# Kernel tuning notes

Hardware: AMD Instinct MI355X
Metric: run time of the kernel (lower is better)

Reference implementation:

```python
import jax, jax.numpy as jnp
import numpy as np

ALPHA = 0.2          # LeakyReLU negative slope
NEG_INF = -9e15      # mask value from the original code


def setup_inputs() -> dict:
    key = jax.random.key(0)
    k1, k2, k3, k4 = jax.random.split(key, 4)
    B, N, F_in, F_out = 8, 2048, 64, 64
    x = jax.random.normal(k1, (B, N, F_in), dtype=jnp.float32)
    adj = jax.random.randint(k2, (B, N, N), 0, 2, dtype=jnp.int32)
    W = jax.random.normal(k3, (F_in, F_out), dtype=jnp.float32)
    a = jax.random.normal(k4, (2 * F_out, 1), dtype=jnp.float32)
    return {"x": x, "adj": adj, "W": W, "a": a}


def reference(x, adj, W, a):
    # h: [B, N, F_out]
    h = jnp.matmul(x, W)
    F_out = W.shape[1]
    a1 = a[:F_out, 0]   # source half of attention vector
    a2 = a[F_out:, 0]   # target half
    # e_ij = leakyrelu(h_i . a1 + h_j . a2)  -- identical math to the
    # original cat([h_i, h_j]) @ a without materializing [B,N*N,2F].
    s1 = jnp.einsum('bnf,f->bn', h, a1)  # [B, N]
    s2 = jnp.einsum('bnf,f->bn', h, a2)  # [B, N]
    e = jax.nn.leaky_relu(s1[:, :, None] + s2[:, None, :], negative_slope=ALPHA)
    masked = jnp.where(adj > 0, e, NEG_INF)
    attention = jax.nn.softmax(masked, axis=2)  # [B, N, N]
    # dropout p=0.0 / eval mode -> identity
    h_prime = jnp.matmul(attention, h)          # [B, N, F_out]
    return jax.nn.elu(h_prime)                  # concat=True branch
```

## Files before the change

### kernel.cpp

```cpp
#include <hip/hip_runtime.h>
#include <cstdint>

#define LRELU_ALPHA 0.2f
#define NEG_INF -9000000000000000.0f
#define L2E 1.4426950408889634f

typedef __bf16 bf16x8 __attribute__((ext_vector_type(8)));
typedef float floatx4 __attribute__((ext_vector_type(4)));

constexpr int Bb = 8, Nn = 2048, Ff = 64;
constexpr int TJ = 64;
constexpr int SEG = 8;
constexpr int SEGJ = Nn / SEG;
constexpr int NROWS = Bb * Nn;
constexpr int LSTR = 264;

__device__ __forceinline__ unsigned f2bf_u(float f) {
    unsigned u = __builtin_bit_cast(unsigned, f);
    return u + 0x7FFFu + ((u >> 16) & 1u);
}
__device__ __forceinline__ unsigned short f2bf(float f) {
    return (unsigned short)(f2bf_u(f) >> 16);
}
__device__ __forceinline__ unsigned pkbf(float lo, float hi) {
    return (f2bf_u(lo) >> 16) | (f2bf_u(hi) & 0xFFFF0000u);
}

__global__ __launch_bounds__(256) void gat_pack(
    const int* __restrict__ adj, unsigned long long* __restrict__ amask)
{
    const int lane = threadIdx.x & 63;
    const int w    = threadIdx.x >> 6;
    const long long wave_id = (long long)blockIdx.x * 4 + w;
    const long long c0 = wave_id * 16;
    #pragma unroll
    for (int it = 0; it < 16; ++it) {
        const long long chunk = c0 + it;
        const int4 v = reinterpret_cast<const int4*>(adj + chunk * 256)[lane];
        const unsigned long long b0 = __ballot(v.x > 0);
        const unsigned long long b1 = __ballot(v.y > 0);
        const unsigned long long b2 = __ballot(v.z > 0);
        const unsigned long long b3 = __ballot(v.w > 0);
        if (lane == 0) {
            ulonglong2* o = reinterpret_cast<ulonglong2*>(amask + chunk * 4);
            o[0] = ulonglong2{b0, b1};
            o[1] = ulonglong2{b2, b3};
        }
    }
}

__global__ __launch_bounds__(256) void gat_prep(
    const float* __restrict__ x, const float* __restrict__ W, const float* __restrict__ a,
    unsigned short* __restrict__ hT, float* __restrict__ s1g, float* __restrict__ s2g)
{
    constexpr int STR2 = 36;
    __shared__ unsigned short hblk[64 * STR2];
    const int tid = threadIdx.x;
    const int blk = blockIdx.x;
    const int b  = blk >> 6;
    const int i0 = (blk & 63) * 32;
    const int w    = tid >> 6;
    const int lane = tid & 63;

    float wcol[64];
    #pragma unroll
    for (int k = 0; k < 64; ++k) wcol[k] = W[k * 64 + lane];
    const float a1 = a[lane], a2 = a[64 + lane];

    for (int r = 0; r < 8; ++r) {
        const int il = w * 8 + r;
        const int i  = i0 + il;
        const float* xrow = x + ((size_t)(b * Nn + i)) * 64;
        float h = 0.f;
        #pragma unroll
        for (int k = 0; k < 64; ++k) h = fmaf(xrow[k], wcol[k], h);
        float p1 = h * a1, p2 = h * a2;
        #pragma unroll
        for (int off = 32; off; off >>= 1) {
            p1 += __shfl_xor(p1, off);
            p2 += __shfl_xor(p2, off);
        }
        if (lane == 0) { s1g[b * Nn + i] = p1 * L2E; s2g[b * Nn + i] = p2 * L2E; }
        hblk[lane * STR2 + il] = f2bf(h);
    }
    __syncthreads();
    {
        const int f = tid >> 2, c = (tid & 3) * 8;
        uint4 v = *reinterpret_cast<const uint4*>(&hblk[f * STR2 + c]);
        *reinterpret_cast<uint4*>(hT + ((size_t)b * 64 + f) * Nn + i0 + c) = v;
    }
}

__global__ __launch_bounds__(256, 4) void gat_attn(
    const unsigned long long* __restrict__ amask, const unsigned short* __restrict__ hT,
    const float* __restrict__ s1g, const float* __restrict__ s2g,
    float* __restrict__ m_part, float* __restrict__ l_part, float* __restrict__ O_part)
{
    __shared__ unsigned short hT_lds[64 * LSTR];
    __shared__ float s2_lds[SEGJ];

    const int tid  = threadIdx.x;
    const int blk  = blockIdx.x;
    const int seg  = blk >> 8;
    const int grp  = blk & 255;
    const int gr0  = grp * 64;
    const int b    = gr0 >> 11;
    const int i0   = gr0 & 2047;
    const int w    = tid >> 6;
    const int lane = tid & 63;
    const int fl   = lane & 15;
    const int q    = lane >> 4;

    const int i = i0 + w * 16 + fl;
    const float s1v = s1g[b * Nn + i];
    const unsigned short* hTb = hT + (size_t)b * 64 * Nn;
    const int jseg0 = seg * SEGJ;

    unsigned long long Bw0, Bw1, Bw2, Bw3;
    {
        const unsigned long long* mrow = amask + (((size_t)(b * Nn + i)) * 8 + seg) * 4;
        ulonglong2 m01 = reinterpret_cast<const ulonglong2*>(mrow)[0];
        ulonglong2 m23 = reinterpret_cast<const ulonglong2*>(mrow)[1];
        Bw0 = m01.x; Bw1 = m01.y; Bw2 = m23.x; Bw3 = m23.y;
    }

    float m = NEG_INF, l = 0.f;
    floatx4 C[4] = {};

    {
        const int fr = tid >> 2;
        const int c0 = (tid & 3) * 64;
        const unsigned short* gsrc = hTb + (size_t)fr * Nn + jseg0 + c0;
        #pragma unroll
        for (int k = 0; k < 8; ++k) {
            uint4 v = reinterpret_cast<const uint4*>(gsrc)[k];
            reinterpret_cast<uint4*>(&hT_lds[fr * LSTR + c0])[k] = v;
        }
        s2_lds[tid] = s2g[b * Nn + jseg0 + tid];
    }
    __syncthreads();

    const int q2 = q * 2;

    auto tile_body = [&](int tloc) {
        unsigned w32[4];
        w32[0] = (unsigned)(Bw0 >> (tloc * 16 + q2));
        w32[1] = (unsigned)(Bw1 >> (tloc * 16 + q2));
        w32[2] = (unsigned)(Bw2 >> (tloc * 16 + q2));
        w32[3] = (unsigned)(Bw3 >> (tloc * 16 + q2));

        float e[16];
        #pragma unroll
        for (int t = 0; t < 2; ++t) {
            float s2v[8];
            *reinterpret_cast<float4*>(&s2v[0]) =
                *reinterpret_cast<const float4*>(&s2_lds[tloc * 64 + t * 32 + q * 8]);
            *reinterpret_cast<float4*>(&s2v[4]) =
                *reinterpret_cast<const float4*>(&s2_lds[tloc * 64 + t * 32 + q * 8 + 4]);
            #pragma unroll
            for (int jj = 0; jj < 8; ++jj) {
                float ev = s1v + s2v[jj];
                ev = fmaxf(ev, LRELU_ALPHA * ev);
                const bool on = (w32[jj & 3] >> (t * 8 + (jj >> 2))) & 1u;
                e[t * 8 + jj] = on ? ev : NEG_INF;
            }
        }
        float tmax = e[0];
        #pragma unroll
        for (int k = 1; k < 16; ++k) tmax = fmaxf(tmax, e[k]);
        tmax = fmaxf(tmax, __shfl_xor(tmax, 16));
        tmax = fmaxf(tmax, __shfl_xor(tmax, 32));
        const float m_new = fmaxf(m, tmax);
        const float alpha_s = exp2f(m - m_new);
        m = m_new;

        float tsum = 0.f, p[16];
        #pragma unroll
        for (int k = 0; k < 16; ++k) {
            p[k] = exp2f(e[k] - m_new);
            tsum += p[k];
        }
        tsum += __shfl_xor(tsum, 16);
        tsum += __shfl_xor(tsum, 32);
        l = l * alpha_s + tsum;

        uint4 pl0, pl1;
        pl0.x = pkbf(p[0], p[1]);  pl0.y = pkbf(p[2], p[3]);
        pl0.z = pkbf(p[4], p[5]);  pl0.w = pkbf(p[6], p[7]);
        pl1.x = pkbf(p[8], p[9]);  pl1.y = pkbf(p[10], p[11]);
        pl1.z = pkbf(p[12], p[13]); pl1.w = pkbf(p[14], p[15]);
        const bf16x8 A0 = __builtin_bit_cast(bf16x8, pl0);
        const bf16x8 A1 = __builtin_bit_cast(bf16x8, pl1);

        float ac[4];
        #pragma unroll
        for (int r = 0; r < 4; ++r) ac[r] = __shfl(alpha_s, q * 4 + r);
        #pragma unroll
        for (int u = 0; u < 4; ++u)
            #pragma unroll
            for (int r = 0; r < 4; ++r) C[u][r] *= ac[r];

        #pragma unroll
        for (int u = 0; u < 4; ++u) {
            const bf16x8 B0 = *reinterpret_cast<const bf16x8*>(
                &hT_lds[(u * 16 + fl) * LSTR + tloc * 64 + q * 8]);
            C[u] = __builtin_amdgcn_mfma_f32_16x16x32_bf16(A0, B0, C[u], 0, 0, 0);
            const bf16x8 B1 = *reinterpret_cast<const bf16x8*>(
                &hT_lds[(u * 16 + fl) * LSTR + tloc * 64 + 32 + q * 8]);
            C[u] = __builtin_amdgcn_mfma_f32_16x16x32_bf16(A1, B1, C[u], 0, 0, 0);
        }
    };

    tile_body(0);
    tile_body(1);
    tile_body(2);
    tile_body(3);

    if (q == 0) {
        const int ri = b * Nn + i;
        m_part[seg * NROWS + ri] = m;
        l_part[seg * NROWS + ri] = l;
    }
    #pragma unroll
    for (int u = 0; u < 4; ++u) {
        #pragma unroll
        for (int r = 0; r < 4; ++r) {
            const int orow = i0 + w * 16 + q * 4 + r;
            O_part[((size_t)seg * NROWS + b * Nn + orow) * 64 + u * 16 + fl] = C[u][r];
        }
    }
}

__global__ __launch_bounds__(256) void gat_merge(
    const float* __restrict__ m_part, const float* __restrict__ l_part,
    const float* __restrict__ O_part, float* __restrict__ out)
{
    const int tid = threadIdx.x;
    const int ri  = blockIdx.x * 4 + (tid >> 6);
    const int f   = tid & 63;

    float mv[SEG];
    #pragma unroll
    for (int s = 0; s < SEG; ++s) mv[s] = m_part[s * NROWS + ri];
    float mstar = mv[0];
    #pragma unroll
    for (int s = 1; s < SEG; ++s) mstar = fmaxf(mstar, mv[s]);

    float lsum = 0.f, acc = 0.f;
    #pragma unroll
    for (int s = 0; s < SEG; ++s) {
        const float wgt = exp2f(mv[s] - mstar);
        lsum += l_part[s * NROWS + ri] * wgt;
        acc  += O_part[((size_t)s * NROWS + ri) * 64 + f] * wgt;
    }
    float v = acc / lsum;
    v = (v > 0.f) ? v : (exp2f(v * L2E) - 1.f);
    out[(size_t)ri * 64 + f] = v;
}

extern "C" void kernel_launch(void* const* d_in, const int* in_sizes, int n_in,
                              void* d_out, int out_size, void* d_ws, size_t ws_size,
                              hipStream_t stream) {
    const float* x   = (const float*)d_in[0];
    const int*   adj = (const int*)d_in[1];
    const float* W   = (const float*)d_in[2];
    const float* a   = (const float*)d_in[3];
    float* out = (float*)d_out;

    char* p = (char*)d_ws;
    unsigned short* hT = (unsigned short*)p;  p += (size_t)Bb * 64 * Nn * sizeof(unsigned short);
    float* s1 = (float*)p;                    p += (size_t)NROWS * sizeof(float);
    float* s2 = (float*)p;                    p += (size_t)NROWS * sizeof(float);
    float* m_part = (float*)p;                p += (size_t)SEG * NROWS * sizeof(float);
    float* l_part = (float*)p;                p += (size_t)SEG * NROWS * sizeof(float);
    float* O_part = (float*)p;                p += (size_t)SEG * NROWS * 64 * sizeof(float);
    unsigned long long* amask = (unsigned long long*)p;

    gat_pack<<<dim3(2048), dim3(256), 0, stream>>>(adj, amask);
    gat_prep<<<dim3(Bb * Nn / 32), dim3(256), 0, stream>>>(x, W, a, hT, s1, s2);
    gat_attn<<<dim3(SEG * (Bb * Nn / 64)), dim3(256), 0, stream>>>(
        amask, hT, s1, s2, m_part, l_part, O_part);
    gat_merge<<<dim3(NROWS / 4), dim3(256), 0, stream>>>(m_part, l_part, O_part, out);
}
```

Measured before the change: 247.7 us.

## Split attention into 16 column segments with one-pass softmax and LDS-staged output

```diff
diff --git a/kernel.cpp b/kernel.cpp
--- a/kernel.cpp
+++ b/kernel.cpp
@@ -9,11 +9,10 @@
 typedef float floatx4 __attribute__((ext_vector_type(4)));
 
 constexpr int Bb = 8, Nn = 2048, Ff = 64;
-constexpr int TJ = 64;
-constexpr int SEG = 8;
+constexpr int SEG = 16;
 constexpr int SEGJ = Nn / SEG;
 constexpr int NROWS = Bb * Nn;
-constexpr int LSTR = 264;
+constexpr int LSTR2 = 136;
 
 __device__ __forceinline__ unsigned f2bf_u(float f) {
     unsigned u = __builtin_bit_cast(unsigned, f);
@@ -32,9 +31,9 @@
     const int lane = threadIdx.x & 63;
     const int w    = threadIdx.x >> 6;
     const long long wave_id = (long long)blockIdx.x * 4 + w;
-    const long long c0 = wave_id * 16;
-    #pragma unroll
-    for (int it = 0; it < 16; ++it) {
+    const long long c0 = wave_id * 8;
+    #pragma unroll
+    for (int it = 0; it < 8; ++it) {
         const long long chunk = c0 + it;
         const int4 v = reinterpret_cast<const int4*>(adj + chunk * 256)[lane];
         const unsigned long long b0 = __ballot(v.x > 0);
@@ -91,13 +90,15 @@
     }
 }
 
-__global__ __launch_bounds__(256, 4) void gat_attn(
+__global__ __launch_bounds__(256, 5) void gat_attn(
     const unsigned long long* __restrict__ amask, const unsigned short* __restrict__ hT,
     const float* __restrict__ s1g, const float* __restrict__ s2g,
     float* __restrict__ m_part, float* __restrict__ l_part, float* __restrict__ O_part)
 {
-    __shared__ unsigned short hT_lds[64 * LSTR];
+    __shared__ __align__(16) char smem[64 * LSTR2 * 2];
     __shared__ float s2_lds[SEGJ];
+    unsigned short* hT_lds = reinterpret_cast<unsigned short*>(smem);
+    float* out_lds = reinterpret_cast<float*>(smem);
 
     const int tid  = threadIdx.x;
     const int blk  = blockIdx.x;
@@ -116,117 +117,106 @@
     const unsigned short* hTb = hT + (size_t)b * 64 * Nn;
     const int jseg0 = seg * SEGJ;
 
-    unsigned long long Bw0, Bw1, Bw2, Bw3;
+    unsigned w32[4];
     {
-        const unsigned long long* mrow = amask + (((size_t)(b * Nn + i)) * 8 + seg) * 4;
+        const unsigned long long* mrow =
+            amask + (size_t)(b * Nn + i) * 32 + (seg >> 1) * 4;
         ulonglong2 m01 = reinterpret_cast<const ulonglong2*>(mrow)[0];
         ulonglong2 m23 = reinterpret_cast<const ulonglong2*>(mrow)[1];
-        Bw0 = m01.x; Bw1 = m01.y; Bw2 = m23.x; Bw3 = m23.y;
-    }
-
-    float m = NEG_INF, l = 0.f;
-    floatx4 C[4] = {};
-
-    {
-        const int fr = tid >> 2;
-        const int c0 = (tid & 3) * 64;
-        const unsigned short* gsrc = hTb + (size_t)fr * Nn + jseg0 + c0;
-        #pragma unroll
-        for (int k = 0; k < 8; ++k) {
-            uint4 v = reinterpret_cast<const uint4*>(gsrc)[k];
-            reinterpret_cast<uint4*>(&hT_lds[fr * LSTR + c0])[k] = v;
-        }
-        s2_lds[tid] = s2g[b * Nn + jseg0 + tid];
-    }
-    __syncthreads();
-
-    const int q2 = q * 2;
-
-    auto tile_body = [&](int tloc) {
-        unsigned w32[4];
-        w32[0] = (unsigned)(Bw0 >> (tloc * 16 + q2));
-        w32[1] = (unsigned)(Bw1 >> (tloc * 16 + q2));
-        w32[2] = (unsigned)(Bw2 >> (tloc * 16 + q2));
-        w32[3] = (unsigned)(Bw3 >> (tloc * 16 + q2));
-
-        float e[16];
-        #pragma unroll
-        for (int t = 0; t < 2; ++t) {
+        const int sh = (seg & 1) * 32 + q * 2;
+        w32[0] = (unsigned)(m01.x >> sh);
+        w32[1] = (unsigned)(m01.y >> sh);
+        w32[2] = (unsigned)(m23.x >> sh);
+        w32[3] = (unsigned)(m23.y >> sh);
+    }
+
+    #pragma unroll
+    for (int k = 0; k < 4; ++k) {
+        const int fr = k * 16 + (tid >> 4);
+        const int c  = (tid & 15) * 8;
+        uint4 v = *reinterpret_cast<const uint4*>(hTb + (size_t)fr * Nn + jseg0 + c);
+        *reinterpret_cast<uint4*>(&hT_lds[fr * LSTR2 + c]) = v;
+    }
+    if (tid < SEGJ) s2_lds[tid] = s2g[b * Nn + jseg0 + tid];
+    __syncthreads();
+
+    float e[32];
+    #pragma unroll
+    for (int T = 0; T < 2; ++T) {
+        #pragma unroll
+        for (int H = 0; H < 2; ++H) {
             float s2v[8];
             *reinterpret_cast<float4*>(&s2v[0]) =
-                *reinterpret_cast<const float4*>(&s2_lds[tloc * 64 + t * 32 + q * 8]);
+                *reinterpret_cast<const float4*>(&s2_lds[T * 64 + H * 32 + q * 8]);
             *reinterpret_cast<float4*>(&s2v[4]) =
-                *reinterpret_cast<const float4*>(&s2_lds[tloc * 64 + t * 32 + q * 8 + 4]);
+                *reinterpret_cast<const float4*>(&s2_lds[T * 64 + H * 32 + q * 8 + 4]);
             #pragma unroll
             for (int jj = 0; jj < 8; ++jj) {
                 float ev = s1v + s2v[jj];
                 ev = fmaxf(ev, LRELU_ALPHA * ev);
-                const bool on = (w32[jj & 3] >> (t * 8 + (jj >> 2))) & 1u;
-                e[t * 8 + jj] = on ? ev : NEG_INF;
+                const bool on = (w32[jj & 3] >> (T * 16 + H * 8 + (jj >> 2))) & 1u;
+                e[T * 16 + H * 8 + jj] = on ? ev : NEG_INF;
             }
         }
-        float tmax = e[0];
-        #pragma unroll
-        for (int k = 1; k < 16; ++k) tmax = fmaxf(tmax, e[k]);
-        tmax = fmaxf(tmax, __shfl_xor(tmax, 16));
-        tmax = fmaxf(tmax, __shfl_xor(tmax, 32));
-        const float m_new = fmaxf(m, tmax);
-        const float alpha_s = exp2f(m - m_new);
-        m = m_new;
-
-        float tsum = 0.f, p[16];
-        #pragma unroll
-        for (int k = 0; k < 16; ++k) {
-            p[k] = exp2f(e[k] - m_new);
-            tsum += p[k];
-        }
-        tsum += __shfl_xor(tsum, 16);
-        tsum += __shfl_xor(tsum, 32);
-        l = l * alpha_s + tsum;
-
+    }
+
+    float m = e[0];
+    #pragma unroll
+    for (int k = 1; k < 32; ++k) m = fmaxf(m, e[k]);
+    m = fmaxf(m, __shfl_xor(m, 16));
+    m = fmaxf(m, __shfl_xor(m, 32));
+
+    float l = 0.f;
+    #pragma unroll
+    for (int k = 0; k < 32; ++k) {
+        e[k] = exp2f(e[k] - m);
+        l += e[k];
+    }
+    l += __shfl_xor(l, 16);
+    l += __shfl_xor(l, 32);
+
+    floatx4 C[4] = {};
+    #pragma unroll
+    for (int T = 0; T < 2; ++T) {
         uint4 pl0, pl1;
-        pl0.x = pkbf(p[0], p[1]);  pl0.y = pkbf(p[2], p[3]);
-        pl0.z = pkbf(p[4], p[5]);  pl0.w = pkbf(p[6], p[7]);
-        pl1.x = pkbf(p[8], p[9]);  pl1.y = pkbf(p[10], p[11]);
-        pl1.z = pkbf(p[12], p[13]); pl1.w = pkbf(p[14], p[15]);
+        pl0.x = pkbf(e[T*16+0], e[T*16+1]);  pl0.y = pkbf(e[T*16+2], e[T*16+3]);
+        pl0.z = pkbf(e[T*16+4], e[T*16+5]);  pl0.w = pkbf(e[T*16+6], e[T*16+7]);
+        pl1.x = pkbf(e[T*16+8], e[T*16+9]);  pl1.y = pkbf(e[T*16+10], e[T*16+11]);
+        pl1.z = pkbf(e[T*16+12], e[T*16+13]); pl1.w = pkbf(e[T*16+14], e[T*16+15]);
         const bf16x8 A0 = __builtin_bit_cast(bf16x8, pl0);
         const bf16x8 A1 = __builtin_bit_cast(bf16x8, pl1);
-
-        float ac[4];
-        #pragma unroll
-        for (int r = 0; r < 4; ++r) ac[r] = __shfl(alpha_s, q * 4 + r);
-        #pragma unroll
-        for (int u = 0; u < 4; ++u)
-            #pragma unroll
-            for (int r = 0; r < 4; ++r) C[u][r] *= ac[r];
-
         #pragma unroll
         for (int u = 0; u < 4; ++u) {
             const bf16x8 B0 = *reinterpret_cast<const bf16x8*>(
-                &hT_lds[(u * 16 + fl) * LSTR + tloc * 64 + q * 8]);
+                &hT_lds[(u * 16 + fl) * LSTR2 + T * 64 + q * 8]);
             C[u] = __builtin_amdgcn_mfma_f32_16x16x32_bf16(A0, B0, C[u], 0, 0, 0);
             const bf16x8 B1 = *reinterpret_cast<const bf16x8*>(
-                &hT_lds[(u * 16 + fl) * LSTR + tloc * 64 + 32 + q * 8]);
+                &hT_lds[(u * 16 + fl) * LSTR2 + T * 64 + 32 + q * 8]);
             C[u] = __builtin_amdgcn_mfma_f32_16x16x32_bf16(A1, B1, C[u], 0, 0, 0);
         }
-    };
-
-    tile_body(0);
-    tile_body(1);
-    tile_body(2);
-    tile_body(3);
+    }
 
     if (q == 0) {
         const int ri = b * Nn + i;
         m_part[seg * NROWS + ri] = m;
         l_part[seg * NROWS + ri] = l;
     }
-    #pragma unroll
-    for (int u = 0; u < 4; ++u) {
-        #pragma unroll
-        for (int r = 0; r < 4; ++r) {
-            const int orow = i0 + w * 16 + q * 4 + r;
-            O_part[((size_t)seg * NROWS + b * Nn + orow) * 64 + u * 16 + fl] = C[u][r];
+
+    __syncthreads();
+    #pragma unroll
+    for (int u = 0; u < 4; ++u)
+        #pragma unroll
+        for (int r = 0; r < 4; ++r)
+            out_lds[(w * 16 + q * 4 + r) * 65 + u * 16 + fl] = C[u][r];
+    __syncthreads();
+    {
+        float* Obase = O_part + ((size_t)seg * NROWS + b * Nn + i0) * 64;
+        #pragma unroll
+        for (int k = 0; k < 4; ++k) {
+            const int row = k * 16 + (tid >> 4);
+            const int c4  = (tid & 15) * 4;
+            float4 v = *reinterpret_cast<const float4*>(&out_lds[row * 65 + c4]);
+            *reinterpret_cast<float4*>(&Obase[(size_t)row * 64 + c4]) = v;
         }
     }
 }
@@ -276,7 +266,7 @@
     float* O_part = (float*)p;                p += (size_t)SEG * NROWS * 64 * sizeof(float);
     unsigned long long* amask = (unsigned long long*)p;
 
-    gat_pack<<<dim3(2048), dim3(256), 0, stream>>>(adj, amask);
+    gat_pack<<<dim3(4096), dim3(256), 0, stream>>>(adj, amask);
     gat_prep<<<dim3(Bb * Nn / 32), dim3(256), 0, stream>>>(x, W, a, hT, s1, s2);
     gat_attn<<<dim3(SEG * (Bb * Nn / 64)), dim3(256), 0, stream>>>(
         amask, hT, s1, s2, m_part, l_part, O_part);
```

After: 256.1 us. 1.03x slower.
